# Performance work log

Measured on AMD Instinct MI355X. Metric: run time of the kernel, lower is better.

## Reference

```python
import jax, jax.numpy as jnp
import numpy as np

N_NODES = 10000
N_EDGES = 320000
D = 128
H = 4
C = 128
L = 2
NEG_SLOPE = 0.2
LN_EPS = 1e-5


def setup_inputs() -> dict:
    key = jax.random.key(0)
    ks = jax.random.split(key, 8)
    x = jax.random.normal(ks[0], (N_NODES, D), dtype=jnp.float32)
    edge_index = jax.random.randint(ks[1], (2, N_EDGES), 0, N_NODES, dtype=jnp.int64)
    # weights scaled ~Glorot to keep attention logits in a sane range
    Wl = jax.random.normal(ks[2], (L, D, H * C), dtype=jnp.float32) * 0.1
    Wr = jax.random.normal(ks[3], (L, D, H * C), dtype=jnp.float32) * 0.1
    att = jax.random.normal(ks[4], (L, H, C), dtype=jnp.float32) * 0.1
    return {
        "x": x,
        "edge_index": edge_index,
        "Wl": Wl,
        "bl": jnp.zeros((L, H * C), jnp.float32),
        "Wr": Wr,
        "br": jnp.zeros((L, H * C), jnp.float32),
        "att": att,
        "bias": jnp.zeros((L, D), jnp.float32),
        "ln_g": jnp.ones((L, D), jnp.float32),
        "ln_b": jnp.zeros((L, D), jnp.float32),
    }


def _gatv2_layer(x, src, dst, Wl, bl, Wr, br, att, b):
    """GATv2Conv (concat=False -> head mean), messages src->dst, softmax over dst."""
    n = x.shape[0]
    xl = (x @ Wl + bl).reshape(n, H, C)  # source transform
    xr = (x @ Wr + br).reshape(n, H, C)  # target transform
    s = jax.nn.leaky_relu(xl[src] + xr[dst], NEG_SLOPE)  # [E, H, C]
    e = jnp.einsum("ehc,hc->eh", s, att)  # attention logits [E, H]
    m = jax.ops.segment_max(e, dst, num_segments=n)  # stable softmax per dst segment
    ex = jnp.exp(e - m[dst])
    denom = jax.ops.segment_sum(ex, dst, num_segments=n)
    alpha = ex / denom[dst]  # [E, H]
    out = jax.ops.segment_sum(alpha[:, :, None] * xl[src], dst, num_segments=n)  # [N, H, C]
    return out.mean(axis=1) + b  # concat=False -> mean over heads, then bias


def _layer_norm(h, g, b):
    mu = h.mean(-1, keepdims=True)
    var = ((h - mu) ** 2).mean(-1, keepdims=True)
    return (h - mu) * jax.lax.rsqrt(var + LN_EPS) * g + b


def reference(x, edge_index, Wl, bl, Wr, br, att, bias, ln_g, ln_b):
    n = x.shape[0]
    loop = jnp.arange(n, dtype=edge_index.dtype)
    src = jnp.concatenate([edge_index[0], loop])  # add self-loops (PyG default)
    dst = jnp.concatenate([edge_index[1], loop])
    for i in range(L):
        h = _gatv2_layer(x, src, dst, Wl[i], bl[i], Wr[i], br[i], att[i], bias[i])
        x = h + x  # residual
        x = jax.nn.relu(_layer_norm(x, ln_g[i], ln_b[i]))
    return x
```

## Files before the change

kernel.cpp:

```cpp
#include <hip/hip_runtime.h>
#include <math.h>

#define N_NODES 10000
#define N_EDGES 320000
#define E_TOT   (N_EDGES + N_NODES)
#define NEG 0.2f
#define CAP 96

typedef short bf16x8 __attribute__((ext_vector_type(8)));
typedef float f32x4 __attribute__((ext_vector_type(4)));
typedef float f32x2 __attribute__((ext_vector_type(2)));

static __device__ __forceinline__ float4 ld4g(const float* p) { return *(const float4*)p; }

static __device__ __forceinline__ uint4 ldg4(const unsigned short* p, unsigned byteoff) {
    return *(const uint4*)((const char*)p + byteoff);
}
static __device__ __forceinline__ int ldgi(const int* p, int e) { return p[e]; }

static __device__ __forceinline__ unsigned short f2b(float f) {
    unsigned u;
    __builtin_memcpy(&u, &f, 4);
    unsigned r = (u + 0x7fffu + ((u >> 16) & 1u)) >> 16;
    return (unsigned short)r;
}
static __device__ __forceinline__ f32x2 unpk(unsigned d) {
    f32x2 r;
    r.x = __uint_as_float(d << 16);
    r.y = __uint_as_float(d & 0xffff0000u);
    return r;
}

template <int CTRL>
static __device__ __forceinline__ float dpp_add_step(float x) {
    int y = __builtin_amdgcn_update_dpp(0, __float_as_int(x), CTRL, 0xf, 0xf, true);
    return x + __int_as_float(y);
}
static __device__ __forceinline__ float row_sum16(float x) {
    x = dpp_add_step<0x121>(x);
    x = dpp_add_step<0x122>(x);
    x = dpp_add_step<0x124>(x);
    x = dpp_add_step<0x128>(x);
    return x;
}

static __device__ __forceinline__ void comp_round(
    uint4 u, bool valid,
    const f32x2* __restrict__ xr2, const f32x2* __restrict__ at2,
    f32x2* __restrict__ acc2, float* __restrict__ dsum) {
    const f32x2 neg2 = {NEG, NEG};
    const unsigned* w = (const unsigned*)&u;
    f32x2 F[4];
#pragma unroll
    for (int q = 0; q < 4; ++q) F[q] = unpk(w[q]);
    f32x2 qq = {0.f, 0.f};
#pragma unroll
    for (int q = 0; q < 4; ++q) {
        f32x2 s = F[q] + xr2[q];
        s = __builtin_elementwise_max(s, s * neg2);
        qq = __builtin_elementwise_fma(s, at2[q], qq);
    }
    float qs = row_sum16(qq.x + qq.y);
    float ev = __expf(qs);
    ev = valid ? ev : 0.f;
    *dsum += ev;
    f32x2 W = {ev, ev};
#pragma unroll
    for (int q = 0; q < 4; ++q)
        acc2[q] = __builtin_elementwise_fma(F[q], W, acc2[q]);
}

__global__ __launch_bounds__(256) void prep_fused_kernel(
    const float* __restrict__ x,
    const float* __restrict__ Wl, const float* __restrict__ Wr,
    unsigned short* __restrict__ xb, unsigned short* __restrict__ WT,
    int* __restrict__ deg) {
    int tid = threadIdx.x, bid = blockIdx.x;
    __shared__ float tbuf[32][33];

    for (int i = bid * 256 + tid; i < N_NODES; i += 256 * 256) deg[i] = 0;

    int l = bid >> 7;
    int rest = bid & 127;
    int ky = rest >> 5, nx = rest & 31;
    int n0 = nx * 32, k0 = ky * 32;
    const float* S = ((n0 < 512) ? Wl : Wr) + (size_t)l * 65536;
    int nn0 = n0 & 511;
    int tx = tid & 31, ty = tid >> 5;
#pragma unroll
    for (int it = 0; it < 4; ++it) {
        int k = k0 + ty + it * 8;
        tbuf[ty + it * 8][tx] = S[(size_t)k * 512 + nn0 + tx];
    }
    __syncthreads();
    unsigned short* dstp = WT + (size_t)l * 1024 * 128;
#pragma unroll
    for (int it = 0; it < 4; ++it) {
        int n = n0 + ty + it * 8;
        int k = k0 + tx;
        dstp[(size_t)n * 128 + k] = f2b(tbuf[tx][ty + it * 8]);
    }
    for (int i = bid * 256 + tid; i < N_NODES * 32; i += 256 * 256) {
        float4 v = ld4g(x + 4 * i);
        ushort4 o = make_ushort4(f2b(v.x), f2b(v.y), f2b(v.z), f2b(v.w));
        *(ushort4*)(xb + 4 * i) = o;
    }
}

template <int DO_FILL>
__global__ __launch_bounds__(256) void gemm_mfma_kernel(const unsigned short* __restrict__ A,
                                                        const unsigned short* __restrict__ Bt,
                                                        const float* __restrict__ bl,
                                                        const float* __restrict__ br,
                                                        unsigned short* __restrict__ xlh,
                                                        unsigned short* __restrict__ xrh,
                                                        const int* __restrict__ ei,
                                                        int* __restrict__ deg,
                                                        int* __restrict__ csr_src) {
    __shared__ unsigned short As[128][72];
    __shared__ unsigned short Bs[128][72];
    int tid = threadIdx.x;
    int wave = tid >> 6, lane = tid & 63;
    int wm = wave >> 1, wn = wave & 1;
    int l15 = lane & 15, quad = lane >> 4;
    int row0 = blockIdx.y * 128, col0 = blockIdx.x * 128;
    const float* bias = (col0 < 512) ? (bl + col0) : (br + col0 - 512);

    f32x4 acc[4][4];
#pragma unroll
    for (int mi = 0; mi < 4; ++mi)
#pragma unroll
        for (int ni = 0; ni < 4; ++ni)
#pragma unroll
            for (int r = 0; r < 4; ++r) acc[mi][ni][r] = 0.f;

#pragma unroll
    for (int kc = 0; kc < 2; ++kc) {
#pragma unroll
        for (int it = 0; it < 4; ++it) {
            int e = tid + it * 256;
            int r = e >> 3, s = e & 7;
            int gr = row0 + r;
            bf16x8 v = (bf16x8)(short)0;
            if (gr < N_NODES) v = *(const bf16x8*)(A + (size_t)gr * 128 + kc * 64 + s * 8);
            *(bf16x8*)&As[r][s * 8] = v;
            bf16x8 w = *(const bf16x8*)(Bt + (size_t)(col0 + r) * 128 + kc * 64 + s * 8);
            *(bf16x8*)&Bs[r][s * 8] = w;
        }
        __syncthreads();
#pragma unroll
        for (int kq = 0; kq < 2; ++kq) {
            bf16x8 af[4], bfr[4];
#pragma unroll
            for (int mi = 0; mi < 4; ++mi)
                af[mi] = *(const bf16x8*)&As[wm * 64 + mi * 16 + l15][kq * 32 + quad * 8];
#pragma unroll
            for (int ni = 0; ni < 4; ++ni)
                bfr[ni] = *(const bf16x8*)&Bs[wn * 64 + ni * 16 + l15][kq * 32 + quad * 8];
#pragma unroll
            for (int mi = 0; mi < 4; ++mi)
#pragma unroll
                for (int ni = 0; ni < 4; ++ni)
                    acc[mi][ni] = __builtin_amdgcn_mfma_f32_16x16x32_bf16(af[mi], bfr[ni], acc[mi][ni], 0, 0, 0);
        }
        __syncthreads();
    }

    float bv[4];
#pragma unroll
    for (int ni = 0; ni < 4; ++ni) bv[ni] = bias[wn * 64 + ni * 16 + l15];

    int h = (col0 >> 7) & 3;
    unsigned short* dstb = ((col0 < 512) ? xlh : xrh) + (((size_t)h * N_NODES) << 7);

#pragma unroll
    for (int mi = 0; mi < 4; ++mi) {
#pragma unroll
        for (int r = 0; r < 4; ++r) {
            int grow = row0 + wm * 64 + mi * 16 + quad * 4 + r;
            if (grow >= N_NODES) continue;
#pragma unroll
            for (int ni = 0; ni < 4; ++ni) {
                int cc = wn * 64 + ni * 16 + l15;
                dstb[((size_t)grow << 7) + cc] = f2b(acc[mi][ni][r] + bv[ni]);
            }
        }
    }

    if (DO_FILL) {
        bool is64 = ((ei[1] | ei[3] | ei[5] | ei[7]) == 0);
        int nthreads = gridDim.x * gridDim.y * 256;
        int gid = (blockIdx.y * gridDim.x + blockIdx.x) * 256 + tid;
        for (int i = gid; i < E_TOT; i += nthreads) {
            int src, dst;
            if (i < N_EDGES) {
                if (is64) { const long long* e = (const long long*)ei; src = (int)e[i]; dst = (int)e[N_EDGES + i]; }
                else { src = ei[i]; dst = ei[N_EDGES + i]; }
            } else {
                src = dst = i - N_EDGES;
            }
            int pos = atomicAdd(&deg[dst], 1);
            if (pos < CAP) csr_src[dst * CAP + pos] = src;
        }
    }
}

__global__ __launch_bounds__(256) void attn_kernel(
    const unsigned short* __restrict__ xlh,
    const unsigned short* __restrict__ xrh,
    const int* __restrict__ deg, const int* __restrict__ csr_src,
    const float* __restrict__ att,
    float* __restrict__ hpart) {
    int tid = threadIdx.x;
    unsigned bid = blockIdx.x;
    int w = tid >> 6, lane = tid & 63;
    int head = (int)((bid & 7u) >> 1);
    int chunk = (int)((bid >> 3) * 2 + (bid & 1u));
    int dst = chunk * 4 + w;
    head = __builtin_amdgcn_readfirstlane(head);
    dst = __builtin_amdgcn_readfirstlane(dst);
    int e = lane >> 4, g = lane & 15;
    unsigned gboff = (unsigned)(g << 4);

    const unsigned short* XL = xlh + (((size_t)head * N_NODES) << 7);

    f32x2 xr2[4], at2[4];
    {
        const unsigned short* xrrow = xrh + (((size_t)head * N_NODES + (size_t)dst) << 7);
        uint4 u = *(const uint4*)(xrrow + g * 8);
        xr2[0] = unpk(u.x); xr2[1] = unpk(u.y); xr2[2] = unpk(u.z); xr2[3] = unpk(u.w);
        const float* ap = att + head * 128 + g * 8;
        float4 a = ld4g(ap);
        float4 b = ld4g(ap + 4);
        at2[0].x = a.x; at2[0].y = a.y; at2[1].x = a.z; at2[1].y = a.w;
        at2[2].x = b.x; at2[2].y = b.y; at2[3].x = b.z; at2[3].y = b.w;
    }

    float d = 0.f;
    f32x2 acc2[4] = {{0.f, 0.f}, {0.f, 0.f}, {0.f, 0.f}, {0.f, 0.f}};

    int len = deg[dst];
    if (len > CAP) len = CAP;
    const int* cp = csr_src + dst * CAP;
    int rounds = (len + 3) >> 2;

    int i1 = (rounds > 1) ? ldgi(cp + 4, e) : 0;
    int i2 = (rounds > 2) ? ldgi(cp + 8, e) : 0;
    int ic0 = (e < len) ? ldgi(cp, e) : 0;
    {
        int raw = ldgi(cp, e);
        ic0 = (e < len) ? raw : 0;
    }
    uint4 uc = ldg4(XL, ((unsigned)ic0 << 8) + gboff);
    uint4 un = uc;

    for (int r = 0; r < rounds; ++r) {
        bool more = (r + 1) < rounds;
        if (more) {
            int vm = len - 4 * (r + 1);
            int icn = (e < vm) ? i1 : 0;
            un = ldg4(XL, ((unsigned)icn << 8) + gboff);
            i1 = i2;
            i2 = ((r + 3) < rounds) ? ldgi(cp + 4 * (r + 3), e) : 0;
        }
        comp_round(uc, e < (len - 4 * r), xr2, at2, acc2, &d);
        uc = un;
    }

    float t[8];
#pragma unroll
    for (int q = 0; q < 4; ++q) { t[2 * q] = acc2[q].x; t[2 * q + 1] = acc2[q].y; }
#pragma unroll
    for (int j = 0; j < 8; ++j) {
        t[j] += __shfl_xor(t[j], 16, 64);
        t[j] += __shfl_xor(t[j], 32, 64);
    }
    d += __shfl_xor(d, 16, 64);
    d += __shfl_xor(d, 32, 64);
    float inv = 1.f / d;
#pragma unroll
    for (int j = 0; j < 8; ++j) t[j] *= inv;

    if (lane < 16) {
        float* op = hpart + (((size_t)head * N_NODES + (size_t)dst) << 7) + g * 8;
        *(float4*)op = make_float4(t[0], t[1], t[2], t[3]);
        *(float4*)(op + 4) = make_float4(t[4], t[5], t[6], t[7]);
    }
}

__global__ __launch_bounds__(256) void combine_kernel(
    const float* __restrict__ hpart, const float* __restrict__ x_in,
    const float* __restrict__ bias, const float* __restrict__ ln_g,
    const float* __restrict__ ln_b, float* __restrict__ x_out,
    unsigned short* __restrict__ xb_out) {
    int wv = (blockIdx.x * blockDim.x + threadIdx.x) >> 6;
    if (wv >= N_NODES) return;
    int lane = threadIdx.x & 63;
    int dst = __builtin_amdgcn_readfirstlane(wv);
    int c = lane * 2;
    const float* hp = hpart + ((size_t)dst << 7) + c;
    const size_t hs = ((size_t)N_NODES) << 7;
    f32x2 h0 = *(const f32x2*)(hp);
    f32x2 h1 = *(const f32x2*)(hp + hs);
    f32x2 h2 = *(const f32x2*)(hp + 2 * hs);
    f32x2 h3 = *(const f32x2*)(hp + 3 * hs);
    f32x2 bi = *(const f32x2*)(bias + c);
    f32x2 xi = *(const f32x2*)(x_in + ((size_t)dst << 7) + c);
    f32x2 hc = ((h0 + h1) + (h2 + h3)) * 0.25f + bi + xi;
    float sm = hc.x + hc.y;
    float sq = hc.x * hc.x + hc.y * hc.y;
    sm = row_sum16(sm); sm += __shfl_xor(sm, 16, 64); sm += __shfl_xor(sm, 32, 64);
    sq = row_sum16(sq); sq += __shfl_xor(sq, 16, 64); sq += __shfl_xor(sq, 32, 64);
    float mu = sm * (1.f / 128.f);
    float var = sq * (1.f / 128.f) - mu * mu;
    float rs = rsqrtf(var + 1e-5f);
    f32x2 gg = *(const f32x2*)(ln_g + c);
    f32x2 bb = *(const f32x2*)(ln_b + c);
    float y0 = fmaxf((hc.x - mu) * rs * gg.x + bb.x, 0.f);
    float y1 = fmaxf((hc.y - mu) * rs * gg.y + bb.y, 0.f);
    f32x2 y = {y0, y1};
    *(f32x2*)(x_out + ((size_t)dst << 7) + c) = y;
    if (xb_out) {
        unsigned pk = ((unsigned)f2b(y0)) | (((unsigned)f2b(y1)) << 16);
        *(unsigned*)(xb_out + ((size_t)dst << 7) + c) = pk;
    }
}

extern "C" void kernel_launch(void* const* d_in, const int* in_sizes, int n_in,
                              void* d_out, int out_size, void* d_ws, size_t ws_size,
                              hipStream_t stream) {
    const float* x    = (const float*)d_in[0];
    const int*   ei   = (const int*)d_in[1];
    const float* Wl   = (const float*)d_in[2];
    const float* bl   = (const float*)d_in[3];
    const float* Wr   = (const float*)d_in[4];
    const float* br   = (const float*)d_in[5];
    const float* att  = (const float*)d_in[6];
    const float* bias = (const float*)d_in[7];
    const float* lng  = (const float*)d_in[8];
    const float* lnb  = (const float*)d_in[9];
    float* out = (float*)d_out;

    char* ws = (char*)d_ws;
    unsigned short* xlh = (unsigned short*)ws; ws += (size_t)4 * N_NODES * 128 * 2;
    unsigned short* xrh = (unsigned short*)ws; ws += (size_t)4 * N_NODES * 128 * 2;
    float* hpart = (float*)ws;          ws += (size_t)4 * N_NODES * 128 * 4;
    float* xbuf  = (float*)ws;          ws += (size_t)N_NODES * 128 * 4;
    unsigned short* xb = (unsigned short*)ws; ws += (size_t)N_NODES * 128 * 2;
    unsigned short* WT = (unsigned short*)ws; ws += (size_t)2 * 1024 * 128 * 2;
    int* deg     = (int*)ws;            ws += (size_t)N_NODES * 4;
    int* csr_src = (int*)ws;            ws += (size_t)N_NODES * CAP * 4;

    prep_fused_kernel<<<256, 256, 0, stream>>>(x, Wl, Wr, xb, WT, deg);

    for (int l = 0; l < 2; ++l) {
        const float* xin = (l == 0) ? x : xbuf;
        float* xout = (l == 0) ? xbuf : out;
        unsigned short* xbo = (l == 0) ? xb : (unsigned short*)nullptr;
        if (l == 0)
            gemm_mfma_kernel<1><<<dim3(8, 79), 256, 0, stream>>>(
                xb, WT, bl, br, xlh, xrh, ei, deg, csr_src);
        else
            gemm_mfma_kernel<0><<<dim3(8, 79), 256, 0, stream>>>(
                xb, WT + (size_t)1024 * 128, bl + 512, br + 512, xlh, xrh, ei, deg, csr_src);
        attn_kernel<<<10000, 256, 0, stream>>>(
            xlh, xrh, deg, csr_src, att + (size_t)l * 512, hpart);
        combine_kernel<<<2500, 256, 0, stream>>>(
            hpart, xin, bias + (size_t)l * 128,
            lng + (size_t)l * 128, lnb + (size_t)l * 128, xout, xbo);
    }
}
```

Measured before the change: 214.2 us.

## Make attention kernel grid-stride over nodes and split full/masked edge rounds

Launches a fixed 2048-block grid where each wave loops over several destination nodes instead of one block per node group, amortizing block launch and per-block setup such as attention vector loads. The edge loop is split into unmasked full rounds of four edges plus a single masked remainder round, removing per-round validity checks. Index prefetching is reduced from two rounds ahead to one, which may expose more gather latency.

After: 216.1 us. Within noise of the previous version (+0.9%).

```diff
diff --git a/kernel.cpp b/kernel.cpp
--- a/kernel.cpp
+++ b/kernel.cpp
@@ -44,7 +44,31 @@
     return x;
 }
 
-static __device__ __forceinline__ void comp_round(
+static __device__ __forceinline__ void comp_full(
+    uint4 u,
+    const f32x2* __restrict__ xr2, const f32x2* __restrict__ at2,
+    f32x2* __restrict__ acc2, float* __restrict__ dsum) {
+    const f32x2 neg2 = {NEG, NEG};
+    const unsigned* w = (const unsigned*)&u;
+    f32x2 F[4];
+#pragma unroll
+    for (int q = 0; q < 4; ++q) F[q] = unpk(w[q]);
+    f32x2 qq = {0.f, 0.f};
+#pragma unroll
+    for (int q = 0; q < 4; ++q) {
+        f32x2 s = F[q] + xr2[q];
+        s = __builtin_elementwise_max(s, s * neg2);
+        qq = __builtin_elementwise_fma(s, at2[q], qq);
+    }
+    float ev = __expf(row_sum16(qq.x + qq.y));
+    *dsum += ev;
+    f32x2 W = {ev, ev};
+#pragma unroll
+    for (int q = 0; q < 4; ++q)
+        acc2[q] = __builtin_elementwise_fma(F[q], W, acc2[q]);
+}
+
+static __device__ __forceinline__ void comp_mask(
     uint4 u, bool valid,
     const f32x2* __restrict__ xr2, const f32x2* __restrict__ at2,
     f32x2* __restrict__ acc2, float* __restrict__ dsum) {
@@ -60,8 +84,7 @@
         s = __builtin_elementwise_max(s, s * neg2);
         qq = __builtin_elementwise_fma(s, at2[q], qq);
     }
-    float qs = row_sum16(qq.x + qq.y);
-    float ev = __expf(qs);
+    float ev = __expf(row_sum16(qq.x + qq.y));
     ev = valid ? ev : 0.f;
     *dsum += ev;
     f32x2 W = {ev, ev};
@@ -214,21 +237,17 @@
     int tid = threadIdx.x;
     unsigned bid = blockIdx.x;
     int w = tid >> 6, lane = tid & 63;
-    int head = (int)((bid & 7u) >> 1);
-    int chunk = (int)((bid >> 3) * 2 + (bid & 1u));
-    int dst = chunk * 4 + w;
-    head = __builtin_amdgcn_readfirstlane(head);
-    dst = __builtin_amdgcn_readfirstlane(dst);
+    int head = __builtin_amdgcn_readfirstlane((int)((bid & 7u) >> 1));
+    int slot = (int)((bid >> 3) * 2 + (bid & 1u));
     int e = lane >> 4, g = lane & 15;
     unsigned gboff = (unsigned)(g << 4);
 
     const unsigned short* XL = xlh + (((size_t)head * N_NODES) << 7);
-
-    f32x2 xr2[4], at2[4];
+    const unsigned short* XR = xrh + (((size_t)head * N_NODES) << 7);
+    float* HP = hpart + (((size_t)head * N_NODES) << 7);
+
+    f32x2 at2[4];
     {
-        const unsigned short* xrrow = xrh + (((size_t)head * N_NODES + (size_t)dst) << 7);
-        uint4 u = *(const uint4*)(xrrow + g * 8);
-        xr2[0] = unpk(u.x); xr2[1] = unpk(u.y); xr2[2] = unpk(u.z); xr2[3] = unpk(u.w);
         const float* ap = att + head * 128 + g * 8;
         float4 a = ld4g(ap);
         float4 b = ld4g(ap + 4);
@@ -236,55 +255,61 @@
         at2[2].x = b.x; at2[2].y = b.y; at2[3].x = b.z; at2[3].y = b.w;
     }
 
-    float d = 0.f;
-    f32x2 acc2[4] = {{0.f, 0.f}, {0.f, 0.f}, {0.f, 0.f}, {0.f, 0.f}};
-
-    int len = deg[dst];
-    if (len > CAP) len = CAP;
-    const int* cp = csr_src + dst * CAP;
-    int rounds = (len + 3) >> 2;
-
-    int i1 = (rounds > 1) ? ldgi(cp + 4, e) : 0;
-    int i2 = (rounds > 2) ? ldgi(cp + 8, e) : 0;
-    int ic0 = (e < len) ? ldgi(cp, e) : 0;
-    {
-        int raw = ldgi(cp, e);
-        ic0 = (e < len) ? raw : 0;
-    }
-    uint4 uc = ldg4(XL, ((unsigned)ic0 << 8) + gboff);
-    uint4 un = uc;
-
-    for (int r = 0; r < rounds; ++r) {
-        bool more = (r + 1) < rounds;
-        if (more) {
-            int vm = len - 4 * (r + 1);
-            int icn = (e < vm) ? i1 : 0;
-            un = ldg4(XL, ((unsigned)icn << 8) + gboff);
-            i1 = i2;
-            i2 = ((r + 3) < rounds) ? ldgi(cp + 4 * (r + 3), e) : 0;
-        }
-        comp_round(uc, e < (len - 4 * r), xr2, at2, acc2, &d);
-        uc = un;
-    }
-
-    float t[8];
-#pragma unroll
-    for (int q = 0; q < 4; ++q) { t[2 * q] = acc2[q].x; t[2 * q + 1] = acc2[q].y; }
-#pragma unroll
-    for (int j = 0; j < 8; ++j) {
-        t[j] += __shfl_xor(t[j], 16, 64);
-        t[j] += __shfl_xor(t[j], 32, 64);
-    }
-    d += __shfl_xor(d, 16, 64);
-    d += __shfl_xor(d, 32, 64);
-    float inv = 1.f / d;
-#pragma unroll
-    for (int j = 0; j < 8; ++j) t[j] *= inv;
-
-    if (lane < 16) {
-        float* op = hpart + (((size_t)head * N_NODES + (size_t)dst) << 7) + g * 8;
-        *(float4*)op = make_float4(t[0], t[1], t[2], t[3]);
-        *(float4*)(op + 4) = make_float4(t[4], t[5], t[6], t[7]);
+    for (int dst0 = slot * 4 + w; dst0 < N_NODES; dst0 += 2048) {
+        int dst = __builtin_amdgcn_readfirstlane(dst0);
+
+        f32x2 xr2[4];
+        {
+            uint4 u = *(const uint4*)(XR + ((size_t)dst << 7) + g * 8);
+            xr2[0] = unpk(u.x); xr2[1] = unpk(u.y); xr2[2] = unpk(u.z); xr2[3] = unpk(u.w);
+        }
+
+        int len = deg[dst];
+        if (len > CAP) len = CAP;
+        const int* cp = csr_src + dst * CAP;
+        int full = len >> 2, rem = len & 3;
+
+        float d = 0.f;
+        f32x2 acc2[4] = {{0.f, 0.f}, {0.f, 0.f}, {0.f, 0.f}, {0.f, 0.f}};
+
+        if (full) {
+            int idx = ldgi(cp, e);
+            uint4 uc = ldg4(XL, ((unsigned)idx << 8) + gboff);
+            for (int r = 0; r + 1 < full; ++r) {
+                int i1 = ldgi(cp + 4 * (r + 1), e);
+                uint4 un = ldg4(XL, ((unsigned)i1 << 8) + gboff);
+                comp_full(uc, xr2, at2, acc2, &d);
+                uc = un;
+            }
+            comp_full(uc, xr2, at2, acc2, &d);
+        }
+        if (rem) {
+            int raw = ldgi(cp + 4 * full, e);
+            int idx = (e < rem) ? raw : 0;
+            uint4 u = ldg4(XL, ((unsigned)idx << 8) + gboff);
+            comp_mask(u, e < rem, xr2, at2, acc2, &d);
+        }
+
+        float t[8];
+#pragma unroll
+        for (int q = 0; q < 4; ++q) { t[2 * q] = acc2[q].x; t[2 * q + 1] = acc2[q].y; }
+#pragma unroll
+        for (int j = 0; j < 8; ++j) {
+            t[j] += __shfl_xor(t[j], 16, 64);
+            t[j] += __shfl_xor(t[j], 32, 64);
+        }
+        float ds = d;
+        ds += __shfl_xor(ds, 16, 64);
+        ds += __shfl_xor(ds, 32, 64);
+        float inv = 1.f / ds;
+#pragma unroll
+        for (int j = 0; j < 8; ++j) t[j] *= inv;
+
+        if (lane < 16) {
+            float* op = HP + ((size_t)dst << 7) + g * 8;
+            *(float4*)op = make_float4(t[0], t[1], t[2], t[3]);
+            *(float4*)(op + 4) = make_float4(t[4], t[5], t[6], t[7]);
+        }
     }
 }
 
@@ -363,7 +388,7 @@
         else
             gemm_mfma_kernel<0><<<dim3(8, 79), 256, 0, stream>>>(
                 xb, WT + (size_t)1024 * 128, bl + 512, br + 512, xlh, xrh, ei, deg, csr_src);
-        attn_kernel<<<10000, 256, 0, stream>>>(
+        attn_kernel<<<2048, 256, 0, stream>>>(
             xlh, xrh, deg, csr_src, att + (size_t)l * 512, hpart);
         combine_kernel<<<2500, 256, 0, stream>>>(
             hpart, xin, bias + (size_t)l * 128,
```
